# Performance work log

Hardware: AMD Instinct MI355X
Metric: run time of the kernel (lower is better)

Reference implementation:

```python
import jax, jax.numpy as jnp
import numpy as np

B, T, C, H = 4, 2048, 1024, 16
HS = C // H  # head_size = 64


def setup_inputs() -> dict:
    key = jax.random.key(0)
    ks = jax.random.split(key, 12)
    s_in = C ** -0.5
    s_ff = (4 * C) ** -0.5
    return {
        "x": jax.random.normal(ks[0], (B, T, C), jnp.float32),
        "Wq": jax.random.normal(ks[1], (H, C, HS), jnp.float32) * s_in,
        "Wk": jax.random.normal(ks[2], (H, C, HS), jnp.float32) * s_in,
        "Wv": jax.random.normal(ks[3], (H, C, HS), jnp.float32) * s_in,
        "Wp": jax.random.normal(ks[4], (C, C), jnp.float32) * s_in,
        "bp": jnp.zeros((C,), jnp.float32),
        "W1": jax.random.normal(ks[5], (C, 4 * C), jnp.float32) * s_in,
        "b1": jnp.zeros((4 * C,), jnp.float32),
        "W2": jax.random.normal(ks[6], (4 * C, C), jnp.float32) * s_ff,
        "b2": jnp.zeros((C,), jnp.float32),
        "g1": jnp.ones((C,), jnp.float32),
        "be1": jnp.zeros((C,), jnp.float32),
        "g2": jnp.ones((C,), jnp.float32),
        "be2": jnp.zeros((C,), jnp.float32),
    }


def _layernorm(x, g, b, eps=1e-5):
    mu = jnp.mean(x, axis=-1, keepdims=True)
    var = jnp.var(x, axis=-1, keepdims=True)
    return (x - mu) * jax.lax.rsqrt(var + eps) * g + b


def reference(x, Wq, Wk, Wv, Wp, bp, W1, b1, W2, b2, g1, be1, g2, be2):
    # NOTE: residuals add to the post-LN tensor (faithful to the torch code),
    # and the attention scale uses C = n_embed, not head_size.
    x1 = _layernorm(x, g1, be1)                       # [B,T,C]
    q = jnp.einsum('btc,hcd->bhtd', x1, Wq)
    k = jnp.einsum('btc,hcd->bhtd', x1, Wk)
    v = jnp.einsum('btc,hcd->bhtd', x1, Wv)
    scores = jnp.einsum('bhtd,bhsd->bhts', q, k) * (C ** -0.5)
    causal = jnp.tril(jnp.ones((T, T), bool))
    scores = jnp.where(causal, scores, -jnp.inf)
    att = jax.nn.softmax(scores, axis=-1)             # [B,H,T,T]
    o = jnp.einsum('bhts,bhsd->bhtd', att, v)
    o = o.transpose(0, 2, 1, 3).reshape(B, T, C)      # concat heads
    x2 = x1 + o @ Wp + bp
    x3 = _layernorm(x2, g2, be2)
    ff = jax.nn.relu(x3 @ W1 + b1) @ W2 + b2
    return x3 + ff
```

## Files before the change

### kernel.cpp

```cpp
#include <hip/hip_runtime.h>
#include <cstdint>

typedef unsigned short u16;
typedef unsigned int u32;
typedef __bf16 bf16x8 __attribute__((ext_vector_type(8)));
typedef float f32x4 __attribute__((ext_vector_type(4)));

#define DEVINL __device__ __forceinline__

DEVINL float bf2f(u16 h) { union { u32 u; float f; } v; v.u = ((u32)h) << 16; return v.f; }
DEVINL u16 f2bf(float f) {
  union { float f; u32 u; } v; v.f = f;
  u32 u = v.u;
  return (u16)((u + 0x7fffu + ((u >> 16) & 1u)) >> 16);
}

DEVINL float fexp2(float x) {
#if __has_builtin(__builtin_amdgcn_exp2f)
  return __builtin_amdgcn_exp2f(x);
#else
  return exp2f(x);
#endif
}

DEVINL void gld_lds16(const void* g, void* l) {
  __builtin_amdgcn_global_load_lds(
      (__attribute__((address_space(1))) void*)(g),
      (__attribute__((address_space(3))) void*)(l), 16, 0, 0);
}

__global__ __launch_bounds__(256) void ktransf(const float* __restrict__ in,
                                               u16* __restrict__ out,
                                               int R, int C, long ibs, long obs) {
  __shared__ __align__(16) u16 tile[64][80];
  const float* ip = in + (long)blockIdx.z * ibs;
  u16* op = out + (long)blockIdx.z * obs;
  int c0 = blockIdx.x * 64, r0 = blockIdx.y * 64;
  int t = threadIdx.x;
#pragma unroll
  for (int ph = 0; ph < 2; ++ph) {
    int ch = ph * 256 + t;
    int r = ch >> 3, cc = (ch & 7) * 8;
    const float* src = &ip[(long)(r0 + r) * C + c0 + cc];
    float4 a = *(const float4*)src;
    float4 b = *(const float4*)(src + 4);
    u16 tmp[8] = {f2bf(a.x), f2bf(a.y), f2bf(a.z), f2bf(a.w),
                  f2bf(b.x), f2bf(b.y), f2bf(b.z), f2bf(b.w)};
    *(uint4*)&tile[r][cc] = *(uint4*)tmp;
  }
  __syncthreads();
#pragma unroll
  for (int ph = 0; ph < 2; ++ph) {
    int ch = ph * 256 + t;
    int c = ch >> 3, rr = (ch & 7) * 8;
    u16 tmp[8];
#pragma unroll
    for (int i = 0; i < 8; ++i) tmp[i] = tile[rr + i][c];
    *(uint4*)&op[(long)(c0 + c) * R + r0 + rr] = *(uint4*)tmp;
  }
}

__global__ __launch_bounds__(256) void ktransb(const u16* __restrict__ in,
                                               u16* __restrict__ out,
                                               int R, int C, long ibs, long obs) {
  __shared__ __align__(16) u16 tile[64][80];
  const u16* ip = in + (long)blockIdx.z * ibs;
  u16* op = out + (long)blockIdx.z * obs;
  int c0 = blockIdx.x * 64, r0 = blockIdx.y * 64;
  int t = threadIdx.x;
#pragma unroll
  for (int ph = 0; ph < 2; ++ph) {
    int ch = ph * 256 + t;
    int r = ch >> 3, cc = (ch & 7) * 8;
    *(uint4*)&tile[r][cc] = *(const uint4*)&ip[(long)(r0 + r) * C + c0 + cc];
  }
  __syncthreads();
#pragma unroll
  for (int ph = 0; ph < 2; ++ph) {
    int ch = ph * 256 + t;
    int c = ch >> 3, rr = (ch & 7) * 8;
    u16 tmp[8];
#pragma unroll
    for (int i = 0; i < 8; ++i) tmp[i] = tile[rr + i][c];
    *(uint4*)&op[(long)(c0 + c) * R + r0 + rr] = *(uint4*)tmp;
  }
}

__global__ __launch_bounds__(256) void kln_f(const float* __restrict__ x,
                                             const float* __restrict__ g,
                                             const float* __restrict__ be,
                                             u16* __restrict__ y) {
  long row = blockIdx.x;
  int t = threadIdx.x;
  float4 xv = *(const float4*)&x[row * 1024 + t * 4];
  float f0 = xv.x, f1 = xv.y, f2 = xv.z, f3 = xv.w;
  float s = f0 + f1 + f2 + f3;
  float s2 = f0 * f0 + f1 * f1 + f2 * f2 + f3 * f3;
#pragma unroll
  for (int off = 32; off >= 1; off >>= 1) {
    s += __shfl_xor(s, off);
    s2 += __shfl_xor(s2, off);
  }
  __shared__ float red[8];
  int w = t >> 6, l = t & 63;
  if (l == 0) { red[w] = s; red[4 + w] = s2; }
  __syncthreads();
  s = red[0] + red[1] + red[2] + red[3];
  s2 = red[4] + red[5] + red[6] + red[7];
  float mu = s * (1.0f / 1024.0f);
  float var = s2 * (1.0f / 1024.0f) - mu * mu;
  float rs = rsqrtf(var + 1e-5f);
  float4 gv = *(const float4*)&g[t * 4];
  float4 bv = *(const float4*)&be[t * 4];
  ushort4 ov;
  ov.x = f2bf((f0 - mu) * rs * gv.x + bv.x);
  ov.y = f2bf((f1 - mu) * rs * gv.y + bv.y);
  ov.z = f2bf((f2 - mu) * rs * gv.z + bv.z);
  ov.w = f2bf((f3 - mu) * rs * gv.w + bv.w);
  *(ushort4*)&y[row * 1024 + t * 4] = ov;
}

__global__ __launch_bounds__(256) void kln_b(const u16* __restrict__ x,
                                             const float* __restrict__ g,
                                             const float* __restrict__ be,
                                             u16* __restrict__ y) {
  long row = blockIdx.x;
  int t = threadIdx.x;
  ushort4 xv = *(const ushort4*)&x[row * 1024 + t * 4];
  float f0 = bf2f(xv.x), f1 = bf2f(xv.y), f2 = bf2f(xv.z), f3 = bf2f(xv.w);
  float s = f0 + f1 + f2 + f3;
  float s2 = f0 * f0 + f1 * f1 + f2 * f2 + f3 * f3;
#pragma unroll
  for (int off = 32; off >= 1; off >>= 1) {
    s += __shfl_xor(s, off);
    s2 += __shfl_xor(s2, off);
  }
  __shared__ float red[8];
  int w = t >> 6, l = t & 63;
  if (l == 0) { red[w] = s; red[4 + w] = s2; }
  __syncthreads();
  s = red[0] + red[1] + red[2] + red[3];
  s2 = red[4] + red[5] + red[6] + red[7];
  float mu = s * (1.0f / 1024.0f);
  float var = s2 * (1.0f / 1024.0f) - mu * mu;
  float rs = rsqrtf(var + 1e-5f);
  float4 gv = *(const float4*)&g[t * 4];
  float4 bv = *(const float4*)&be[t * 4];
  ushort4 ov;
  ov.x = f2bf((f0 - mu) * rs * gv.x + bv.x);
  ov.y = f2bf((f1 - mu) * rs * gv.y + bv.y);
  ov.z = f2bf((f2 - mu) * rs * gv.z + bv.z);
  ov.w = f2bf((f3 - mu) * rs * gv.w + bv.w);
  *(ushort4*)&y[row * 1024 + t * 4] = ov;
}

template <int EPI, int OF32>
__global__ __launch_bounds__(256) void kgemm(const u16* __restrict__ A,
                                             const u16* __restrict__ BT, int K,
                                             const float* __restrict__ bias,
                                             const u16* __restrict__ resid,
                                             void* __restrict__ outv, int ldc) {
  __shared__ __align__(16) u16 sA[128 * 64];
  __shared__ __align__(16) u16 sB[128 * 64];
  int tid = threadIdx.x;
  int l = tid & 63, wv = tid >> 6;
  int wm = (wv >> 1) * 64, wn = (wv & 1) * 64;
  long m0 = (long)blockIdx.y * 128, n0 = (long)blockIdx.x * 128;
  const u16* Ab = A + m0 * K;
  const u16* Bb = BT + n0 * K;
  f32x4 acc[4][4] = {};

  for (int k0 = 0; k0 < K; k0 += 64) {
    __syncthreads();
#pragma unroll
    for (int it = 0; it < 4; ++it) {
      int c = it * 256 + tid;
      int r = c >> 3;
      int k8 = (c & 7) ^ (r & 7);
      gld_lds16(Ab + (long)r * K + k0 + k8 * 8, &sA[c * 8]);
    }
#pragma unroll
    for (int it = 0; it < 4; ++it) {
      int c = it * 256 + tid;
      int r = c >> 3;
      int k8 = (c & 7) ^ (r & 7);
      gld_lds16(Bb + (long)r * K + k0 + k8 * 8, &sB[c * 8]);
    }
    __syncthreads();
#pragma unroll
    for (int kk = 0; kk < 2; ++kk) {
      int k8 = kk * 4 + (l >> 4);
      bf16x8 af[4], bfr[4];
#pragma unroll
      for (int mi = 0; mi < 4; ++mi) {
        int r = wm + mi * 16 + (l & 15);
        af[mi] = *(const bf16x8*)&sA[(r * 8 + (k8 ^ (r & 7))) * 8];
      }
#pragma unroll
      for (int ni = 0; ni < 4; ++ni) {
        int r = wn + ni * 16 + (l & 15);
        bfr[ni] = *(const bf16x8*)&sB[(r * 8 + (k8 ^ (r & 7))) * 8];
      }
#pragma unroll
      for (int mi = 0; mi < 4; ++mi)
#pragma unroll
        for (int ni = 0; ni < 4; ++ni)
          acc[mi][ni] =
              __builtin_amdgcn_mfma_f32_16x16x32_bf16(af[mi], bfr[ni], acc[mi][ni], 0, 0, 0);
    }
  }
#pragma unroll
  for (int mi = 0; mi < 4; ++mi) {
#pragma unroll
    for (int ni = 0; ni < 4; ++ni) {
#pragma unroll
      for (int j = 0; j < 4; ++j) {
        long row = m0 + wm + mi * 16 + (l >> 4) * 4 + j;
        long col = n0 + wn + ni * 16 + (l & 15);
        float v = acc[mi][ni][j];
        if constexpr (EPI == 0) {
          long tn = col >> 10, jj = col & 1023;
          long hh = jj >> 6, dd = jj & 63;
          long bb = row >> 11, tt = row & 2047;
          if (tn == 0) v *= 0.045084220027780106f;
          ((u16*)outv)[(((tn * 4 + bb) * 16 + hh) * 2048 + tt) * 64 + dd] = f2bf(v);
        } else {
          v += bias[col];
          if constexpr (EPI == 2) v = fmaxf(v, 0.0f);
          if constexpr (EPI == 1) v += bf2f(resid[row * ldc + col]);
          if constexpr (OF32) ((float*)outv)[row * ldc + col] = v;
          else ((u16*)outv)[row * ldc + col] = f2bf(v);
        }
      }
    }
  }
}

__global__ __launch_bounds__(256) void kattn(const u16* __restrict__ q,
                                             const u16* __restrict__ kmat,
                                             const u16* __restrict__ vt,
                                             u16* __restrict__ o) {
  __shared__ __align__(16) u16 Ks[64 * 64];
  __shared__ __align__(16) u16 Vs[64 * 64];
  __shared__ __align__(16) u16 Ps[4 * 32 * 64];
  int bh = blockIdx.x;
  int qi = (gridDim.y - 1) - blockIdx.y;
  int tid = threadIdx.x, w = tid >> 6, l = tid & 63;
  long bQ = (long)bh * 2048 * 64;
  int qrow0 = qi * 128 + w * 32;
  const float NEGINF = -__builtin_inff();

  bf16x8 qf[2][2];
#pragma unroll
  for (int mi = 0; mi < 2; ++mi)
#pragma unroll
    for (int kk = 0; kk < 2; ++kk) {
      int tt = qrow0 + mi * 16 + (l & 15);
      int kd = kk * 32 + (l >> 4) * 8;
      qf[mi][kk] = *(const bf16x8*)&q[bQ + (long)tt * 64 + kd];
    }
  f32x4 ao[2][4] = {};
  float mr[2][4], lr[2][4];
#pragma unroll
  for (int mi = 0; mi < 2; ++mi)
#pragma unroll
    for (int j = 0; j < 4; ++j) { mr[mi][j] = NEGINF; lr[mi][j] = 0.f; }

  u16* Pw = &Ps[w * 2048];
  int njt = qi * 2 + 2;
  for (int jt = 0; jt < njt; ++jt) {
    int s0 = jt * 64;
    bool skip = (s0 > qrow0 + 31);
    bool need_mask = (s0 + 63 > qrow0);
    __syncthreads();
#pragma unroll
    for (int it = 0; it < 2; ++it) {
      int c = it * 256 + tid;
      int r = c >> 3;
      int k8 = (c & 7) ^ (r & 7);
      gld_lds16(&kmat[bQ + (long)(s0 + r) * 64 + k8 * 8], &Ks[c * 8]);
    }
#pragma unroll
    for (int it = 0; it < 2; ++it) {
      int c = it * 256 + tid;
      int r = c >> 3;
      int s8 = (c & 7) ^ (r & 7);
      gld_lds16(&vt[bQ + (long)r * 2048 + s0 + s8 * 8], &Vs[c * 8]);
    }
    __syncthreads();
    if (skip) continue;
    f32x4 sc[2][4] = {};
#pragma unroll
    for (int kk = 0; kk < 2; ++kk) {
      int k8 = kk * 4 + (l >> 4);
      bf16x8 kf[4];
#pragma unroll
      for (int ni = 0; ni < 4; ++ni) {
        int r = ni * 16 + (l & 15);
        kf[ni] = *(const bf16x8*)&Ks[(r * 8 + (k8 ^ (r & 7))) * 8];
      }
#pragma unroll
      for (int mi = 0; mi < 2; ++mi)
#pragma unroll
        for (int ni = 0; ni < 4; ++ni)
          sc[mi][ni] =
              __builtin_amdgcn_mfma_f32_16x16x32_bf16(qf[mi][kk], kf[ni], sc[mi][ni], 0, 0, 0);
    }
#pragma unroll
    for (int mi = 0; mi < 2; ++mi) {
#pragma unroll
      for (int j = 0; j < 4; ++j) {
        int tg = qrow0 + mi * 16 + (l >> 4) * 4 + j;
        float rmax = NEGINF;
        if (need_mask) {
#pragma unroll
          for (int ni = 0; ni < 4; ++ni) {
            int sg = s0 + ni * 16 + (l & 15);
            float vv = sc[mi][ni][j];
            vv = (sg <= tg) ? vv : NEGINF;
            sc[mi][ni][j] = vv;
            rmax = fmaxf(rmax, vv);
          }
        } else {
#pragma unroll
          for (int ni = 0; ni < 4; ++ni) rmax = fmaxf(rmax, sc[mi][ni][j]);
        }
#pragma unroll
        for (int off = 8; off >= 1; off >>= 1) rmax = fmaxf(rmax, __shfl_xor(rmax, off));
        float mnew = fmaxf(mr[mi][j], rmax);
        float alpha = fexp2(mr[mi][j] - mnew);
        float rsum = 0.f;
#pragma unroll
        for (int ni = 0; ni < 4; ++ni) {
          float p = fexp2(sc[mi][ni][j] - mnew);
          sc[mi][ni][j] = p;
          rsum += p;
        }
#pragma unroll
        for (int off = 8; off >= 1; off >>= 1) rsum += __shfl_xor(rsum, off);
        lr[mi][j] = lr[mi][j] * alpha + rsum;
        mr[mi][j] = mnew;
#pragma unroll
        for (int nd = 0; nd < 4; ++nd) ao[mi][nd][j] *= alpha;
      }
    }
#pragma unroll
    for (int mi = 0; mi < 2; ++mi)
#pragma unroll
      for (int ni = 0; ni < 4; ++ni)
#pragma unroll
        for (int j = 0; j < 4; ++j) {
          int r = mi * 16 + (l >> 4) * 4 + j;
          int cc = ni * 16 + (l & 15);
          Pw[(r * 8 + ((cc >> 3) ^ (r & 7))) * 8 + (cc & 7)] = f2bf(sc[mi][ni][j]);
        }
#pragma unroll
    for (int kk = 0; kk < 2; ++kk) {
      int s8 = kk * 4 + (l >> 4);
      bf16x8 pf[2], vf[4];
#pragma unroll
      for (int mi = 0; mi < 2; ++mi) {
        int r = mi * 16 + (l & 15);
        pf[mi] = *(const bf16x8*)&Pw[(r * 8 + (s8 ^ (r & 7))) * 8];
      }
#pragma unroll
      for (int nd = 0; nd < 4; ++nd) {
        int r = nd * 16 + (l & 15);
        vf[nd] = *(const bf16x8*)&Vs[(r * 8 + (s8 ^ (r & 7))) * 8];
      }
#pragma unroll
      for (int mi = 0; mi < 2; ++mi)
#pragma unroll
        for (int nd = 0; nd < 4; ++nd)
          ao[mi][nd] =
              __builtin_amdgcn_mfma_f32_16x16x32_bf16(pf[mi], vf[nd], ao[mi][nd], 0, 0, 0);
    }
  }
  int b = bh >> 4, h = bh & 15;
#pragma unroll
  for (int mi = 0; mi < 2; ++mi)
#pragma unroll
    for (int nd = 0; nd < 4; ++nd)
#pragma unroll
      for (int j = 0; j < 4; ++j) {
        int tt = qrow0 + mi * 16 + (l >> 4) * 4 + j;
        int dd = nd * 16 + (l & 15);
        float v = ao[mi][nd][j] / lr[mi][j];
        o[((long)(b * 2048 + tt)) * 1024 + h * 64 + dd] = f2bf(v);
      }
}

extern "C" void kernel_launch(void* const* d_in, const int* in_sizes, int n_in,
                              void* d_out, int out_size, void* d_ws, size_t ws_size,
                              hipStream_t stream) {
  const float* x = (const float*)d_in[0];
  const float* Wq = (const float*)d_in[1];
  const float* Wk = (const float*)d_in[2];
  const float* Wv = (const float*)d_in[3];
  const float* Wp = (const float*)d_in[4];
  const float* bp = (const float*)d_in[5];
  const float* W1 = (const float*)d_in[6];
  const float* b1 = (const float*)d_in[7];
  const float* W2 = (const float*)d_in[8];
  const float* b2 = (const float*)d_in[9];
  const float* g1 = (const float*)d_in[10];
  const float* be1 = (const float*)d_in[11];
  const float* g2 = (const float*)d_in[12];
  const float* be2 = (const float*)d_in[13];

  u16* ws = (u16*)d_ws;
  u16* wqkvT = ws;
  u16* wpT = wqkvT + 3145728;
  u16* w1T = wpT + 1048576;
  u16* w2T = w1T + 4194304;
  u16* qb = w2T + 4194304;
  u16* kb = qb + 8388608;
  u16* vb = kb + 8388608;
  u16* vtb = vb + 8388608;
  u16* ob = vtb + 8388608;
  u16* x1 = ob + 8388608;
  float* outp = (float*)d_out;
  u16* x2 = vb;
  u16* x3 = ob;
  u16* hb = qb;

  ktransf<<<dim3(1, 16, 16), 256, 0, stream>>>(Wq, wqkvT, 1024, 64, 65536, 65536);
  ktransf<<<dim3(1, 16, 16), 256, 0, stream>>>(Wk, wqkvT + 1048576, 1024, 64, 65536, 65536);
  ktransf<<<dim3(1, 16, 16), 256, 0, stream>>>(Wv, wqkvT + 2097152, 1024, 64, 65536, 65536);
  ktransf<<<dim3(16, 16, 1), 256, 0, stream>>>(Wp, wpT, 1024, 1024, 0, 0);
  ktransf<<<dim3(64, 16, 1), 256, 0, stream>>>(W1, w1T, 1024, 4096, 0, 0);
  ktransf<<<dim3(16, 64, 1), 256, 0, stream>>>(W2, w2T, 4096, 1024, 0, 0);

  kln_f<<<8192, 256, 0, stream>>>(x, g1, be1, x1);
  kgemm<0, 0><<<dim3(24, 64), 256, 0, stream>>>(x1, wqkvT, 1024, nullptr, nullptr, qb, 0);
  ktransb<<<dim3(1, 32, 64), 256, 0, stream>>>(vb, vtb, 2048, 64, 131072, 131072);
  kattn<<<dim3(64, 16), 256, 0, stream>>>(qb, kb, vtb, ob);
  kgemm<1, 0><<<dim3(8, 64), 256, 0, stream>>>(ob, wpT, 1024, bp, x1, x2, 1024);
  kln_b<<<8192, 256, 0, stream>>>(x2, g2, be2, x3);
  kgemm<2, 0><<<dim3(32, 64), 256, 0, stream>>>(x3, w1T, 1024, b1, nullptr, hb, 4096);
  kgemm<1, 1><<<dim3(8, 64), 256, 0, stream>>>(hb, w2T, 4096, b2, x3, outp, 1024);
}
```

Baseline: 472.3 us.

## Double-buffer K/V tiles in attention to overlap loads with compute

The K and V shared-memory tiles in the causal attention kernel get two buffers. The next tile's global-to-LDS loads are issued before the current tile's QK^T, softmax and PV work, and a single barrier per iteration replaces the previous two. This is meant to hide global load latency behind MFMA and softmax work. It raises LDS use per block from about 32KB to 48KB, which can lower the number of resident blocks per CU.

New measurement: 473.3 us. No clear change (+0.2%).

```diff
diff --git a/kernel.cpp b/kernel.cpp
--- a/kernel.cpp
+++ b/kernel.cpp
@@ -240,8 +240,8 @@
                                              const u16* __restrict__ kmat,
                                              const u16* __restrict__ vt,
                                              u16* __restrict__ o) {
-  __shared__ __align__(16) u16 Ks[64 * 64];
-  __shared__ __align__(16) u16 Vs[64 * 64];
+  __shared__ __align__(16) u16 Ks[2][64 * 64];
+  __shared__ __align__(16) u16 Vs[2][64 * 64];
   __shared__ __align__(16) u16 Ps[4 * 32 * 64];
   int bh = blockIdx.x;
   int qi = (gridDim.y - 1) - blockIdx.y;
@@ -268,113 +268,140 @@
 
   u16* Pw = &Ps[w * 2048];
   int njt = qi * 2 + 2;
-  for (int jt = 0; jt < njt; ++jt) {
-    int s0 = jt * 64;
-    bool skip = (s0 > qrow0 + 31);
-    bool need_mask = (s0 + 63 > qrow0);
-    __syncthreads();
+
+  {
 #pragma unroll
     for (int it = 0; it < 2; ++it) {
       int c = it * 256 + tid;
       int r = c >> 3;
       int k8 = (c & 7) ^ (r & 7);
-      gld_lds16(&kmat[bQ + (long)(s0 + r) * 64 + k8 * 8], &Ks[c * 8]);
+      gld_lds16(&kmat[bQ + (long)r * 64 + k8 * 8], &Ks[0][c * 8]);
     }
 #pragma unroll
     for (int it = 0; it < 2; ++it) {
       int c = it * 256 + tid;
       int r = c >> 3;
       int s8 = (c & 7) ^ (r & 7);
-      gld_lds16(&vt[bQ + (long)r * 2048 + s0 + s8 * 8], &Vs[c * 8]);
+      gld_lds16(&vt[bQ + (long)r * 2048 + s8 * 8], &Vs[0][c * 8]);
+    }
+  }
+  __syncthreads();
+
+  int cur = 0;
+  for (int jt = 0; jt < njt; ++jt) {
+    int s0 = jt * 64;
+    if (jt + 1 < njt) {
+      int s1 = s0 + 64;
+      int nb = cur ^ 1;
+#pragma unroll
+      for (int it = 0; it < 2; ++it) {
+        int c = it * 256 + tid;
+        int r = c >> 3;
+        int k8 = (c & 7) ^ (r & 7);
+        gld_lds16(&kmat[bQ + (long)(s1 + r) * 64 + k8 * 8], &Ks[nb][c * 8]);
+      }
+#pragma unroll
+      for (int it = 0; it < 2; ++it) {
+        int c = it * 256 + tid;
+        int r = c >> 3;
+        int s8 = (c & 7) ^ (r & 7);
+        gld_lds16(&vt[bQ + (long)r * 2048 + s1 + s8 * 8], &Vs[nb][c * 8]);
+      }
+    }
+    bool skip = (s0 > qrow0 + 31);
+    bool need_mask = (s0 + 63 > qrow0);
+    if (!skip) {
+      const u16* Kc = Ks[cur];
+      const u16* Vc = Vs[cur];
+      f32x4 sc[2][4] = {};
+#pragma unroll
+      for (int kk = 0; kk < 2; ++kk) {
+        int k8 = kk * 4 + (l >> 4);
+        bf16x8 kf[4];
+#pragma unroll
+        for (int ni = 0; ni < 4; ++ni) {
+          int r = ni * 16 + (l & 15);
+          kf[ni] = *(const bf16x8*)&Kc[(r * 8 + (k8 ^ (r & 7))) * 8];
+        }
+#pragma unroll
+        for (int mi = 0; mi < 2; ++mi)
+#pragma unroll
+          for (int ni = 0; ni < 4; ++ni)
+            sc[mi][ni] =
+                __builtin_amdgcn_mfma_f32_16x16x32_bf16(qf[mi][kk], kf[ni], sc[mi][ni], 0, 0, 0);
+      }
+#pragma unroll
+      for (int mi = 0; mi < 2; ++mi) {
+#pragma unroll
+        for (int j = 0; j < 4; ++j) {
+          int tg = qrow0 + mi * 16 + (l >> 4) * 4 + j;
+          float rmax = NEGINF;
+          if (need_mask) {
+#pragma unroll
+            for (int ni = 0; ni < 4; ++ni) {
+              int sg = s0 + ni * 16 + (l & 15);
+              float vv = sc[mi][ni][j];
+              vv = (sg <= tg) ? vv : NEGINF;
+              sc[mi][ni][j] = vv;
+              rmax = fmaxf(rmax, vv);
+            }
+          } else {
+#pragma unroll
+            for (int ni = 0; ni < 4; ++ni) rmax = fmaxf(rmax, sc[mi][ni][j]);
+          }
+#pragma unroll
+          for (int off = 8; off >= 1; off >>= 1) rmax = fmaxf(rmax, __shfl_xor(rmax, off));
+          float mnew = fmaxf(mr[mi][j], rmax);
+          float alpha = fexp2(mr[mi][j] - mnew);
+          float rsum = 0.f;
+#pragma unroll
+          for (int ni = 0; ni < 4; ++ni) {
+            float p = fexp2(sc[mi][ni][j] - mnew);
+            sc[mi][ni][j] = p;
+            rsum += p;
+          }
+#pragma unroll
+          for (int off = 8; off >= 1; off >>= 1) rsum += __shfl_xor(rsum, off);
+          lr[mi][j] = lr[mi][j] * alpha + rsum;
+          mr[mi][j] = mnew;
+#pragma unroll
+          for (int nd = 0; nd < 4; ++nd) ao[mi][nd][j] *= alpha;
+        }
+      }
+#pragma unroll
+      for (int mi = 0; mi < 2; ++mi)
+#pragma unroll
+        for (int ni = 0; ni < 4; ++ni)
+#pragma unroll
+          for (int j = 0; j < 4; ++j) {
+            int r = mi * 16 + (l >> 4) * 4 + j;
+            int cc = ni * 16 + (l & 15);
+            Pw[(r * 8 + ((cc >> 3) ^ (r & 7))) * 8 + (cc & 7)] = f2bf(sc[mi][ni][j]);
+          }
+#pragma unroll
+      for (int kk = 0; kk < 2; ++kk) {
+        int s8 = kk * 4 + (l >> 4);
+        bf16x8 pf[2], vf[4];
+#pragma unroll
+        for (int mi = 0; mi < 2; ++mi) {
+          int r = mi * 16 + (l & 15);
+          pf[mi] = *(const bf16x8*)&Pw[(r * 8 + (s8 ^ (r & 7))) * 8];
+        }
+#pragma unroll
+        for (int nd = 0; nd < 4; ++nd) {
+          int r = nd * 16 + (l & 15);
+          vf[nd] = *(const bf16x8*)&Vc[(r * 8 + (s8 ^ (r & 7))) * 8];
+        }
+#pragma unroll
+        for (int mi = 0; mi < 2; ++mi)
+#pragma unroll
+          for (int nd = 0; nd < 4; ++nd)
+            ao[mi][nd] =
+                __builtin_amdgcn_mfma_f32_16x16x32_bf16(pf[mi], vf[nd], ao[mi][nd], 0, 0, 0);
+      }
     }
     __syncthreads();
-    if (skip) continue;
-    f32x4 sc[2][4] = {};
-#pragma unroll
-    for (int kk = 0; kk < 2; ++kk) {
-      int k8 = kk * 4 + (l >> 4);
-      bf16x8 kf[4];
-#pragma unroll
-      for (int ni = 0; ni < 4; ++ni) {
-        int r = ni * 16 + (l & 15);
-        kf[ni] = *(const bf16x8*)&Ks[(r * 8 + (k8 ^ (r & 7))) * 8];
-      }
-#pragma unroll
-      for (int mi = 0; mi < 2; ++mi)
-#pragma unroll
-        for (int ni = 0; ni < 4; ++ni)
-          sc[mi][ni] =
-              __builtin_amdgcn_mfma_f32_16x16x32_bf16(qf[mi][kk], kf[ni], sc[mi][ni], 0, 0, 0);
-    }
-#pragma unroll
-    for (int mi = 0; mi < 2; ++mi) {
-#pragma unroll
-      for (int j = 0; j < 4; ++j) {
-        int tg = qrow0 + mi * 16 + (l >> 4) * 4 + j;
-        float rmax = NEGINF;
-        if (need_mask) {
-#pragma unroll
-          for (int ni = 0; ni < 4; ++ni) {
-            int sg = s0 + ni * 16 + (l & 15);
-            float vv = sc[mi][ni][j];
-            vv = (sg <= tg) ? vv : NEGINF;
-            sc[mi][ni][j] = vv;
-            rmax = fmaxf(rmax, vv);
-          }
-        } else {
-#pragma unroll
-          for (int ni = 0; ni < 4; ++ni) rmax = fmaxf(rmax, sc[mi][ni][j]);
-        }
-#pragma unroll
-        for (int off = 8; off >= 1; off >>= 1) rmax = fmaxf(rmax, __shfl_xor(rmax, off));
-        float mnew = fmaxf(mr[mi][j], rmax);
-        float alpha = fexp2(mr[mi][j] - mnew);
-        float rsum = 0.f;
-#pragma unroll
-        for (int ni = 0; ni < 4; ++ni) {
-          float p = fexp2(sc[mi][ni][j] - mnew);
-          sc[mi][ni][j] = p;
-          rsum += p;
-        }
-#pragma unroll
-        for (int off = 8; off >= 1; off >>= 1) rsum += __shfl_xor(rsum, off);
-        lr[mi][j] = lr[mi][j] * alpha + rsum;
-        mr[mi][j] = mnew;
-#pragma unroll
-        for (int nd = 0; nd < 4; ++nd) ao[mi][nd][j] *= alpha;
-      }
-    }
-#pragma unroll
-    for (int mi = 0; mi < 2; ++mi)
-#pragma unroll
-      for (int ni = 0; ni < 4; ++ni)
-#pragma unroll
-        for (int j = 0; j < 4; ++j) {
-          int r = mi * 16 + (l >> 4) * 4 + j;
-          int cc = ni * 16 + (l & 15);
-          Pw[(r * 8 + ((cc >> 3) ^ (r & 7))) * 8 + (cc & 7)] = f2bf(sc[mi][ni][j]);
-        }
-#pragma unroll
-    for (int kk = 0; kk < 2; ++kk) {
-      int s8 = kk * 4 + (l >> 4);
-      bf16x8 pf[2], vf[4];
-#pragma unroll
-      for (int mi = 0; mi < 2; ++mi) {
-        int r = mi * 16 + (l & 15);
-        pf[mi] = *(const bf16x8*)&Pw[(r * 8 + (s8 ^ (r & 7))) * 8];
-      }
-#pragma unroll
-      for (int nd = 0; nd < 4; ++nd) {
-        int r = nd * 16 + (l & 15);
-        vf[nd] = *(const bf16x8*)&Vs[(r * 8 + (s8 ^ (r & 7))) * 8];
-      }
-#pragma unroll
-      for (int mi = 0; mi < 2; ++mi)
-#pragma unroll
-        for (int nd = 0; nd < 4; ++nd)
-          ao[mi][nd] =
-              __builtin_amdgcn_mfma_f32_16x16x32_bf16(pf[mi], vf[nd], ao[mi][nd], 0, 0, 0);
-    }
+    cur ^= 1;
   }
   int b = bh >> 4, h = bh & 15;
 #pragma unroll
```
